# Kernel optimization log

Measured on AMD Instinct MI355X. Metric: run time of the kernel, lower is better.

Reference implementation:

```python
import jax, jax.numpy as jnp
import numpy as np

B, S, D = 2, 2048, 768
H = 12
HD = D // H


def setup_inputs() -> dict:
    key = jax.random.key(0)
    ks = jax.random.split(key, 9)
    s_in = 1.0 / np.sqrt(D)
    return {
        "x": jax.random.normal(ks[0], (B, S, D), dtype=jnp.float32),
        "wq": jax.random.normal(ks[1], (D, D), dtype=jnp.float32) * s_in,
        "bq": jax.random.normal(ks[2], (D,), dtype=jnp.float32) * 0.01,
        "wk": jax.random.normal(ks[3], (D, D), dtype=jnp.float32) * s_in,
        "bk": jax.random.normal(ks[4], (D,), dtype=jnp.float32) * 0.01,
        "wv": jax.random.normal(ks[5], (D, D), dtype=jnp.float32) * s_in,
        "bv": jax.random.normal(ks[6], (D,), dtype=jnp.float32) * 0.01,
        "wo": jax.random.normal(ks[7], (D, D), dtype=jnp.float32) * s_in,
        "bo": jax.random.normal(ks[8], (D,), dtype=jnp.float32) * 0.01,
    }


def reference(x, wq, bq, wk, bk, wv, bv, wo, bo):
    b, s, _ = x.shape
    # projections -> [b, h, s, hd]
    def proj(w, bias):
        return (x @ w + bias).reshape(b, s, H, HD).transpose(0, 2, 1, 3)
    q = proj(wq, bq)
    k = proj(wk, bk)
    v = proj(wv, bv)
    scores = jnp.einsum("bhqd,bhkd->bhqk", q, k)
    causal = jnp.triu(jnp.ones((s, s), dtype=bool), k=1)
    scores = jnp.where(causal, -jnp.inf, scores)
    attn = jax.nn.softmax(scores / np.sqrt(HD), axis=-1)
    # dropout p=0.0 -> identity
    ctx = jnp.einsum("bhqk,bhkd->bhqd", attn, v)
    ctx = ctx.transpose(0, 2, 1, 3).reshape(b, s, D)
    return ctx @ wo + bo
```

## Files before the change

### kernel.cpp

```cpp
#include <hip/hip_runtime.h>
#include <math.h>

#define BB  2
#define SS  2048
#define DD  768
#define HH  12
#define HDD 64
#define BSR (BB * SS)
#define NQT (SS / 64)

typedef __attribute__((ext_vector_type(8))) short bf16x8;
typedef __attribute__((ext_vector_type(4))) float f32x4;
typedef __attribute__((ext_vector_type(4))) int  i32x4;

__device__ inline f32x4 mfma16(bf16x8 a, bf16x8 b, f32x4 c) {
    return __builtin_amdgcn_mfma_f32_16x16x32_bf16(a, b, c, 0, 0, 0);
}

__device__ inline unsigned short f2b(float f) {
    unsigned int u = __float_as_uint(f);
    u += 0x7FFFu + ((u >> 16) & 1u);
    return (unsigned short)(u >> 16);
}
__device__ inline float b2f(unsigned short u) {
    return __uint_as_float((unsigned int)u << 16);
}

__device__ inline void async_copy16(void* lds, const void* g) {
    __builtin_amdgcn_global_load_lds(
        (const __attribute__((address_space(1))) unsigned int*)g,
        (__attribute__((address_space(3))) unsigned int*)lds, 16, 0, 0);
}

__global__ __launch_bounds__(256) void conv_x_kernel(
    const float* __restrict__ x, unsigned short* __restrict__ xb)
{
    int id = blockIdx.x * 256 + threadIdx.x;
    size_t base = (size_t)id * 8;
    float4 a = *(const float4*)&x[base];
    float4 b = *(const float4*)&x[base + 4];
    unsigned short o[8] = {f2b(a.x), f2b(a.y), f2b(a.z), f2b(a.w),
                           f2b(b.x), f2b(b.y), f2b(b.z), f2b(b.w)};
    *(i32x4*)&xb[base] = *(const i32x4*)o;
}

__global__ __launch_bounds__(256) void conv_wT_kernel(
    const float* __restrict__ w0, const float* __restrict__ w1,
    const float* __restrict__ w2, const float* __restrict__ w3,
    unsigned short* __restrict__ o0, unsigned short* __restrict__ o1,
    unsigned short* __restrict__ o2, unsigned short* __restrict__ o3)
{
    const float* w = (blockIdx.z == 0) ? w0 : (blockIdx.z == 1) ? w1
                   : (blockIdx.z == 2) ? w2 : w3;
    unsigned short* o = (blockIdx.z == 0) ? o0 : (blockIdx.z == 1) ? o1
                      : (blockIdx.z == 2) ? o2 : o3;
    const int n0 = blockIdx.x * 64;
    const int k0 = blockIdx.y * 64;
    const int tid = threadIdx.x;

    __shared__ unsigned short tile[64][72];

#pragma unroll
    for (int p = 0; p < 4; ++p) {
        int c  = p * 256 + tid;
        int kr = c >> 4;
        int nc = (c & 15) * 4;
        float4 v = *(const float4*)&w[(size_t)(k0 + kr) * DD + n0 + nc];
        tile[nc + 0][kr] = f2b(v.x);
        tile[nc + 1][kr] = f2b(v.y);
        tile[nc + 2][kr] = f2b(v.z);
        tile[nc + 3][kr] = f2b(v.w);
    }
    __syncthreads();
#pragma unroll
    for (int p = 0; p < 2; ++p) {
        int c  = p * 256 + tid;
        int nr = c >> 3;
        int kc = (c & 7) * 8;
        *(i32x4*)&o[(size_t)(n0 + nr) * DD + k0 + kc] = *(const i32x4*)&tile[nr][kc];
    }
}

__device__ inline void mainloop_64x128(
    const unsigned short* __restrict__ A, const unsigned short* __restrict__ Bt,
    unsigned short (*As)[64], unsigned short (*Bs)[64],
    f32x4 acc[2][4], int m0, int n0, int tid, int mh, int nh, int l16, int quad)
{
    const int swz = l16 & 7;
    for (int k0 = 0; k0 < DD; k0 += 64) {
        __syncthreads();
#pragma unroll
        for (int p = 0; p < 2; ++p) {
            int c  = p * 256 + tid;
            int r  = c >> 3;
            int ch = (c & 7) ^ (r & 7);
            async_copy16(&As[r][(c & 7) * 8], &A[(size_t)(m0 + r) * DD + k0 + ch * 8]);
        }
#pragma unroll
        for (int p = 0; p < 4; ++p) {
            int c  = p * 256 + tid;
            int r  = c >> 3;
            int ch = (c & 7) ^ (r & 7);
            async_copy16(&Bs[r][(c & 7) * 8], &Bt[(size_t)(n0 + r) * DD + k0 + ch * 8]);
        }
        __syncthreads();
        bf16x8 af0[2], af1[2], bf0[4], bf1[4];
#pragma unroll
        for (int mt = 0; mt < 2; ++mt) {
            int r = mh * 32 + mt * 16 + l16;
            af0[mt] = *(const bf16x8*)&As[r][((quad    ) ^ swz) * 8];
            af1[mt] = *(const bf16x8*)&As[r][((quad + 4) ^ swz) * 8];
        }
#pragma unroll
        for (int nt = 0; nt < 4; ++nt) {
            int r = nh * 64 + nt * 16 + l16;
            bf0[nt] = *(const bf16x8*)&Bs[r][((quad    ) ^ swz) * 8];
            bf1[nt] = *(const bf16x8*)&Bs[r][((quad + 4) ^ swz) * 8];
        }
#pragma unroll
        for (int mt = 0; mt < 2; ++mt)
#pragma unroll
            for (int nt = 0; nt < 4; ++nt) {
                acc[mt][nt] = mfma16(af0[mt], bf0[nt], acc[mt][nt]);
                acc[mt][nt] = mfma16(af1[mt], bf1[nt], acc[mt][nt]);
            }
    }
}

__global__ __launch_bounds__(256) void qkv_gemm_kernel(
    const unsigned short* __restrict__ xb,
    const unsigned short* __restrict__ wqT, const unsigned short* __restrict__ wkT,
    const unsigned short* __restrict__ wvT,
    const float* __restrict__ bq, const float* __restrict__ bk,
    const float* __restrict__ bv,
    unsigned short* __restrict__ Qg, unsigned short* __restrict__ Kg,
    unsigned short* __restrict__ Vg)
{
    const int which = blockIdx.z;
    const unsigned short* Bt = (which == 0) ? wqT : (which == 1) ? wkT : wvT;
    const float* bias        = (which == 0) ? bq  : (which == 1) ? bk  : bv;
    unsigned short* out      = (which == 0) ? Qg  : (which == 1) ? Kg  : Vg;

    const int m0 = blockIdx.x * 64;
    const int n0 = blockIdx.y * 128;
    const int tid  = threadIdx.x;
    const int w    = tid >> 6;
    const int lane = tid & 63;
    const int quad = lane >> 4;
    const int l16  = lane & 15;
    const int mh   = w & 1;
    const int nh   = w >> 1;

    __shared__ unsigned short smem[12288];
    unsigned short (*As)[64]  = (unsigned short(*)[64])smem;
    unsigned short (*Bs)[64]  = (unsigned short(*)[64])(smem + 4096);
    unsigned short (*T)[136]  = (unsigned short(*)[136])smem;

    f32x4 zero = {0.f, 0.f, 0.f, 0.f};
    f32x4 acc[2][4];
#pragma unroll
    for (int i = 0; i < 2; ++i)
#pragma unroll
        for (int j = 0; j < 4; ++j) acc[i][j] = zero;

    mainloop_64x128(xb, Bt, As, Bs, acc, m0, n0, tid, mh, nh, l16, quad);

    __syncthreads();

    if (which < 2) {
#pragma unroll
        for (int nt = 0; nt < 4; ++nt) {
            const int col = nh * 64 + nt * 16 + l16;
            const float bvv = bias[n0 + col];
#pragma unroll
            for (int mt = 0; mt < 2; ++mt)
#pragma unroll
                for (int r = 0; r < 4; ++r)
                    T[mh * 32 + mt * 16 + quad * 4 + r][col] =
                        f2b(acc[mt][nt][r] + bvv);
        }
        __syncthreads();
#pragma unroll
        for (int p2 = 0; p2 < 4; ++p2) {
            int c    = p2 * 256 + tid;
            int row  = c >> 4;
            int ck   = c & 15;
            int head = ck >> 3;
            int wi   = ck & 7;
            int sg   = m0 + row;
            int bi   = sg >> 11, si = sg & 2047;
            int hcol = (n0 >> 6) + head;
            *(i32x4*)&out[(((size_t)(bi * HH + hcol)) * SS + si) * HDD + wi * 8] =
                *(const i32x4*)&T[row][head * 64 + wi * 8];
        }
    } else {
        for (int pass = 0; pass < 2; ++pass) {
            if (pass) __syncthreads();
            if (nh == pass) {
#pragma unroll
                for (int nt = 0; nt < 4; ++nt) {
                    const float bvv = bias[n0 + pass * 64 + nt * 16 + l16];
#pragma unroll
                    for (int mt = 0; mt < 2; ++mt) {
                        ushort4 pk;
                        pk.x = f2b(acc[mt][nt][0] + bvv);
                        pk.y = f2b(acc[mt][nt][1] + bvv);
                        pk.z = f2b(acc[mt][nt][2] + bvv);
                        pk.w = f2b(acc[mt][nt][3] + bvv);
                        *(ushort4*)&T[nt * 16 + l16][mh * 32 + mt * 16 + quad * 4] = pk;
                    }
                }
            }
            __syncthreads();
            const int bi   = m0 >> 11;
            const int s0   = m0 & 2047;
            const int hcol = (n0 >> 6) + pass;
#pragma unroll
            for (int p2 = 0; p2 < 2; ++p2) {
                int c    = p2 * 256 + tid;
                int drow = c >> 3;
                int wi   = c & 7;
                *(i32x4*)&out[(((size_t)(bi * HH + hcol)) * HDD + drow) * SS + s0 + wi * 8] =
                    *(const i32x4*)&T[drow][wi * 8];
            }
        }
    }
}

__global__ __launch_bounds__(256) void out_gemm_kernel(
    const unsigned short* __restrict__ cb, const unsigned short* __restrict__ woT,
    const float* __restrict__ bo, float* __restrict__ out)
{
    const int m0 = blockIdx.x * 64;
    const int n0 = blockIdx.y * 128;
    const int tid  = threadIdx.x;
    const int w    = tid >> 6;
    const int lane = tid & 63;
    const int quad = lane >> 4;
    const int l16  = lane & 15;
    const int mh   = w & 1;
    const int nh   = w >> 1;

    __shared__ unsigned short As[64][64];
    __shared__ unsigned short Bs[128][64];

    f32x4 zero = {0.f, 0.f, 0.f, 0.f};
    f32x4 acc[2][4];
#pragma unroll
    for (int i = 0; i < 2; ++i)
#pragma unroll
        for (int j = 0; j < 4; ++j) acc[i][j] = zero;

    mainloop_64x128(cb, woT, As, Bs, acc, m0, n0, tid, mh, nh, l16, quad);

#pragma unroll
    for (int nt = 0; nt < 4; ++nt) {
        const int n = n0 + nh * 64 + nt * 16 + l16;
        const float bvv = bo[n];
#pragma unroll
        for (int mt = 0; mt < 2; ++mt) {
            const int mbase = m0 + mh * 32 + mt * 16 + quad * 4;
#pragma unroll
            for (int r = 0; r < 4; ++r)
                out[(size_t)(mbase + r) * DD + n] = acc[mt][nt][r] + bvv;
        }
    }
}

__global__ __launch_bounds__(256, 3) void attn_mfma_kernel(
    const unsigned short* __restrict__ Qg, const unsigned short* __restrict__ Kg,
    const unsigned short* __restrict__ Vg, unsigned short* __restrict__ Opart,
    float* __restrict__ Mb, float* __restrict__ Lb)
{
    const int sp = blockIdx.x & 1;
    const int qt = (NQT - 1) - (blockIdx.x >> 1);
    const int h  = blockIdx.y;
    const int b  = blockIdx.z;
    const int tid  = threadIdx.x;
    const int w    = tid >> 6;
    const int lane = tid & 63;
    const int quad = lane >> 4;
    const int l16  = lane & 15;
    const int q0   = qt * 64;

    const size_t bh = (size_t)(b * HH + h);
    const unsigned short* qp = Qg + bh * SS * HDD;
    const unsigned short* kp = Kg + bh * SS * HDD;
    const unsigned short* vp = Vg + bh * HDD * SS;

    unsigned short* op = Opart + ((size_t)sp * BB * HH + bh) * SS * HDD;
    float* mp = Mb + ((size_t)sp * BB * HH + bh) * SS;
    float* lp = Lb + ((size_t)sp * BB * HH + bh) * SS;

    const int nT  = qt + 1;
    const int mid = (nT + 1) >> 1;
    const int lo  = sp ? mid : 0;
    const int hi  = sp ? nT  : mid;

    const int query = q0 + w * 16 + l16;

    if (lo >= hi) {
        if (quad == 0) { mp[query] = -INFINITY; lp[query] = 0.f; }
        i32x4 z4 = {0, 0, 0, 0};
#pragma unroll
        for (int p2 = 0; p2 < 2; ++p2) {
            int c = p2 * 64 + lane;
            int row = c >> 3, dc = c & 7;
            *(i32x4*)&op[(size_t)(q0 + w * 16 + row) * HDD + dc * 8] = z4;
        }
        return;
    }

    __shared__ unsigned short Ks[2][64][72];
    __shared__ unsigned short Vt[2][64][72];
    __shared__ unsigned short PsT[4][16][72];
    unsigned short* slab = &PsT[w][0][0];

    const bf16x8 qb0 = *(const bf16x8*)&qp[(size_t)query * HDD + quad * 8];
    const bf16x8 qb1 = *(const bf16x8*)&qp[(size_t)query * HDD + 32 + quad * 8];

    const int pr = tid >> 3;
    const int po = (tid & 7) * 8;

    i32x4 kpre[2], vpre[2];
#pragma unroll
    for (int p = 0; p < 2; ++p) {
        int r = pr + p * 32;
        kpre[p] = *(const i32x4*)&kp[(size_t)(lo * 64 + r) * HDD + po];
        vpre[p] = *(const i32x4*)&vp[(size_t)r * SS + lo * 64 + po];
    }
#pragma unroll
    for (int p = 0; p < 2; ++p) {
        int r = pr + p * 32;
        *(i32x4*)&Ks[0][r][po] = kpre[p];
        *(i32x4*)&Vt[0][r][po] = vpre[p];
    }
    if (lo + 1 < hi) {
#pragma unroll
        for (int p = 0; p < 2; ++p) {
            int r = pr + p * 32;
            kpre[p] = *(const i32x4*)&kp[(size_t)((lo + 1) * 64 + r) * HDD + po];
            vpre[p] = *(const i32x4*)&vp[(size_t)r * SS + (lo + 1) * 64 + po];
        }
    }

    f32x4 zero = {0.f, 0.f, 0.f, 0.f};
    f32x4 o_acc[4];
    float m_i = -INFINITY, l_i = 0.f;
#pragma unroll
    for (int i = 0; i < 4; ++i) o_acc[i] = zero;

    for (int kt = lo; kt < hi; ++kt) {
        const int cbuf = (kt - lo) & 1;
        const int k0   = kt * 64;
        __syncthreads();

        if (kt + 1 < hi) {
#pragma unroll
            for (int p = 0; p < 2; ++p) {
                int r = pr + p * 32;
                *(i32x4*)&Ks[cbuf ^ 1][r][po] = kpre[p];
                *(i32x4*)&Vt[cbuf ^ 1][r][po] = vpre[p];
            }
        }
        if (kt + 2 < hi) {
            const int kn = (kt + 2) * 64;
#pragma unroll
            for (int p = 0; p < 2; ++p) {
                int r = pr + p * 32;
                kpre[p] = *(const i32x4*)&kp[(size_t)(kn + r) * HDD + po];
                vpre[p] = *(const i32x4*)&vp[(size_t)r * SS + kn + po];
            }
        }

        f32x4 s_acc[4];
#pragma unroll
        for (int t = 0; t < 4; ++t) {
            bf16x8 klo = *(const bf16x8*)&Ks[cbuf][t * 16 + l16][quad * 8];
            bf16x8 khi = *(const bf16x8*)&Ks[cbuf][t * 16 + l16][32 + quad * 8];
            s_acc[t] = mfma16(klo, qb0, zero);
            s_acc[t] = mfma16(khi, qb1, s_acc[t]);
        }

        float ps[4][4];
        float mx = -INFINITY;
#pragma unroll
        for (int t = 0; t < 4; ++t)
#pragma unroll
            for (int r = 0; r < 4; ++r) {
                const int key = k0 + t * 16 + quad * 4 + r;
                float val = s_acc[t][r] * 0.125f;
                if (kt == qt && key > query) val = -INFINITY;
                ps[t][r] = val;
                mx = fmaxf(mx, val);
            }
        mx = fmaxf(mx, __shfl_xor(mx, 16));
        mx = fmaxf(mx, __shfl_xor(mx, 32));
        const float mnew  = fmaxf(m_i, mx);
        const float alpha = __expf(m_i - mnew);
        float lsum = 0.f;
#pragma unroll
        for (int t = 0; t < 4; ++t)
#pragma unroll
            for (int r = 0; r < 4; ++r) {
                float pv = __expf(ps[t][r] - mnew);
                ps[t][r] = pv;
                lsum += pv;
            }
        lsum += __shfl_xor(lsum, 16);
        lsum += __shfl_xor(lsum, 32);
        l_i = l_i * alpha + lsum;
        m_i = mnew;
#pragma unroll
        for (int t = 0; t < 4; ++t)
#pragma unroll
            for (int r = 0; r < 4; ++r) o_acc[t][r] *= alpha;

#pragma unroll
        for (int t = 0; t < 4; ++t) {
            ushort4 pk;
            pk.x = f2b(ps[t][0]);
            pk.y = f2b(ps[t][1]);
            pk.z = f2b(ps[t][2]);
            pk.w = f2b(ps[t][3]);
            *(ushort4*)&slab[l16 * 72 + t * 16 + quad * 4] = pk;
        }
        bf16x8 pb0 = *(const bf16x8*)&slab[l16 * 72 + quad * 8];
        bf16x8 pb1 = *(const bf16x8*)&slab[l16 * 72 + 32 + quad * 8];

#pragma unroll
        for (int t2 = 0; t2 < 4; ++t2) {
            bf16x8 vlo = *(const bf16x8*)&Vt[cbuf][t2 * 16 + l16][quad * 8];
            bf16x8 vhi = *(const bf16x8*)&Vt[cbuf][t2 * 16 + l16][32 + quad * 8];
            o_acc[t2] = mfma16(vlo, pb0, o_acc[t2]);
            o_acc[t2] = mfma16(vhi, pb1, o_acc[t2]);
        }
    }

    if (quad == 0) { mp[query] = m_i; lp[query] = l_i; }
#pragma unroll
    for (int t2 = 0; t2 < 4; ++t2) {
        ushort4 pk;
        pk.x = f2b(o_acc[t2][0]);
        pk.y = f2b(o_acc[t2][1]);
        pk.z = f2b(o_acc[t2][2]);
        pk.w = f2b(o_acc[t2][3]);
        *(ushort4*)&slab[l16 * 72 + t2 * 16 + quad * 4] = pk;
    }
#pragma unroll
    for (int p2 = 0; p2 < 2; ++p2) {
        int c   = p2 * 64 + lane;
        int row = c >> 3, dc = c & 7;
        *(i32x4*)&op[(size_t)(q0 + w * 16 + row) * HDD + dc * 8] =
            *(const i32x4*)&slab[row * 72 + dc * 8];
    }
}

__global__ __launch_bounds__(256) void merge_kernel(
    const unsigned short* __restrict__ Opart, const float* __restrict__ Mb,
    const float* __restrict__ Lb, unsigned short* __restrict__ cb)
{
    const int qt  = blockIdx.x;
    const int bhn = blockIdx.y;
    const int b   = bhn / HH, h = bhn % HH;
    const int tid = threadIdx.x;
    const int row = tid >> 2;
    const int d0  = (tid & 3) * 16;
    const int q   = qt * 64 + row;

    const size_t base0 = (size_t)bhn * SS;
    const size_t base1 = ((size_t)BB * HH + bhn) * SS;

    float m0 = Mb[base0 + q], m1 = Mb[base1 + q];
    float l0 = Lb[base0 + q], l1 = Lb[base1 + q];
    float M  = fmaxf(m0, m1);
    float w0 = __expf(m0 - M), w1 = __expf(m1 - M);
    float inv = 1.0f / (w0 * l0 + w1 * l1);
    w0 *= inv; w1 *= inv;

    const unsigned short* o0 = Opart + (base0 + q) * HDD + d0;
    const unsigned short* o1 = Opart + (base1 + q) * HDD + d0;
    unsigned short res[16];
#pragma unroll
    for (int i = 0; i < 16; ++i)
        res[i] = f2b(w0 * b2f(o0[i]) + w1 * b2f(o1[i]));
    unsigned short* dst = &cb[((size_t)(b * SS + q)) * DD + h * HDD + d0];
    *(i32x4*)&dst[0] = *(const i32x4*)&res[0];
    *(i32x4*)&dst[8] = *(const i32x4*)&res[8];
}

extern "C" void kernel_launch(void* const* d_in, const int* in_sizes, int n_in,
                              void* d_out, int out_size, void* d_ws, size_t ws_size,
                              hipStream_t stream)
{
    const float* x  = (const float*)d_in[0];
    const float* wq = (const float*)d_in[1];
    const float* bq = (const float*)d_in[2];
    const float* wk = (const float*)d_in[3];
    const float* bk = (const float*)d_in[4];
    const float* wv = (const float*)d_in[5];
    const float* bv = (const float*)d_in[6];
    const float* wo = (const float*)d_in[7];
    const float* bo = (const float*)d_in[8];
    float* out = (float*)d_out;

    char* p = (char*)d_ws;
    const size_t XB = (size_t)BSR * DD * 2;
    const size_t WB = (size_t)DD * DD * 2;
    const size_t MLB = (size_t)2 * BB * HH * SS * 4;
    unsigned short* xb  = (unsigned short*)p;            p += XB;
    unsigned short* wqT = (unsigned short*)p;            p += WB;
    unsigned short* wkT = (unsigned short*)p;            p += WB;
    unsigned short* wvT = (unsigned short*)p;            p += WB;
    unsigned short* woT = (unsigned short*)p;            p += WB;
    unsigned short* Qg  = (unsigned short*)p;            p += XB;
    unsigned short* Kg  = (unsigned short*)p;            p += XB;
    unsigned short* Vg  = (unsigned short*)p;            p += XB;
    unsigned short* cb  = (unsigned short*)p;            p += XB;
    unsigned short* Opart = (unsigned short*)p;          p += 2 * XB;
    float* Mb = (float*)p;                               p += MLB;
    float* Lb = (float*)p;                               p += MLB;

    conv_x_kernel<<<BSR * DD / (256 * 8), 256, 0, stream>>>(x, xb);
    conv_wT_kernel<<<dim3(DD / 64, DD / 64, 4), 256, 0, stream>>>(
        wq, wk, wv, wo, wqT, wkT, wvT, woT);
    qkv_gemm_kernel<<<dim3(BSR / 64, DD / 128, 3), 256, 0, stream>>>(
        xb, wqT, wkT, wvT, bq, bk, bv, Qg, Kg, Vg);
    attn_mfma_kernel<<<dim3(NQT * 2, HH, BB), 256, 0, stream>>>(
        Qg, Kg, Vg, Opart, Mb, Lb);
    merge_kernel<<<dim3(NQT, BB * HH), 256, 0, stream>>>(Opart, Mb, Lb, cb);
    out_gemm_kernel<<<dim3(BSR / 64, DD / 128), 256, 0, stream>>>(cb, woT, bo, out);
}
```

Baseline: 181.0 us.

## Single-buffer swizzled K/V LDS tiles, fold softmax scale into Q, raise occupancy

The attention kernel's K/V shared-memory tiles become single-buffered with an XOR swizzle instead of padded double buffers. This shrinks LDS use so the launch bound can request 6 blocks per CU instead of 3. The 1/sqrt(hd) scale moves into the Q projection epilogue, removing a multiply per score. The cost is an extra barrier per key tile and prefetch only one tile ahead, so more latency must be hidden by the extra occupancy, and Q is now rounded to bf16 after scaling.

```diff
diff --git a/kernel.cpp b/kernel.cpp
--- a/kernel.cpp
+++ b/kernel.cpp
@@ -140,6 +140,7 @@
     const unsigned short* Bt = (which == 0) ? wqT : (which == 1) ? wkT : wvT;
     const float* bias        = (which == 0) ? bq  : (which == 1) ? bk  : bv;
     unsigned short* out      = (which == 0) ? Qg  : (which == 1) ? Kg  : Vg;
+    const float qs           = (which == 0) ? 0.125f : 1.0f;
 
     const int m0 = blockIdx.x * 64;
     const int n0 = blockIdx.y * 128;
@@ -177,7 +178,7 @@
 #pragma unroll
                 for (int r = 0; r < 4; ++r)
                     T[mh * 32 + mt * 16 + quad * 4 + r][col] =
-                        f2b(acc[mt][nt][r] + bvv);
+                        f2b((acc[mt][nt][r] + bvv) * qs);
         }
         __syncthreads();
 #pragma unroll
@@ -267,7 +268,7 @@
     }
 }
 
-__global__ __launch_bounds__(256, 3) void attn_mfma_kernel(
+__global__ __launch_bounds__(256, 6) void attn_mfma_kernel(
     const unsigned short* __restrict__ Qg, const unsigned short* __restrict__ Kg,
     const unsigned short* __restrict__ Vg, unsigned short* __restrict__ Opart,
     float* __restrict__ Mb, float* __restrict__ Lb)
@@ -311,37 +312,25 @@
         return;
     }
 
-    __shared__ unsigned short Ks[2][64][72];
-    __shared__ unsigned short Vt[2][64][72];
+    __shared__ unsigned short Ks[64][64];
+    __shared__ unsigned short Vt[64][64];
     __shared__ unsigned short PsT[4][16][72];
     unsigned short* slab = &PsT[w][0][0];
 
     const bf16x8 qb0 = *(const bf16x8*)&qp[(size_t)query * HDD + quad * 8];
     const bf16x8 qb1 = *(const bf16x8*)&qp[(size_t)query * HDD + 32 + quad * 8];
 
-    const int pr = tid >> 3;
-    const int po = (tid & 7) * 8;
+    const int pr  = tid >> 3;
+    const int po8 = tid & 7;
+    const int fs  = l16 & 7;
 
     i32x4 kpre[2], vpre[2];
 #pragma unroll
     for (int p = 0; p < 2; ++p) {
-        int r = pr + p * 32;
-        kpre[p] = *(const i32x4*)&kp[(size_t)(lo * 64 + r) * HDD + po];
-        vpre[p] = *(const i32x4*)&vp[(size_t)r * SS + lo * 64 + po];
-    }
-#pragma unroll
-    for (int p = 0; p < 2; ++p) {
-        int r = pr + p * 32;
-        *(i32x4*)&Ks[0][r][po] = kpre[p];
-        *(i32x4*)&Vt[0][r][po] = vpre[p];
-    }
-    if (lo + 1 < hi) {
-#pragma unroll
-        for (int p = 0; p < 2; ++p) {
-            int r = pr + p * 32;
-            kpre[p] = *(const i32x4*)&kp[(size_t)((lo + 1) * 64 + r) * HDD + po];
-            vpre[p] = *(const i32x4*)&vp[(size_t)r * SS + (lo + 1) * 64 + po];
-        }
+        int r  = pr + p * 32;
+        int gc = (po8 ^ (r & 7)) * 8;
+        kpre[p] = *(const i32x4*)&kp[(size_t)(lo * 64 + r) * HDD + gc];
+        vpre[p] = *(const i32x4*)&vp[(size_t)r * SS + lo * 64 + gc];
     }
 
     f32x4 zero = {0.f, 0.f, 0.f, 0.f};
@@ -351,33 +340,33 @@
     for (int i = 0; i < 4; ++i) o_acc[i] = zero;
 
     for (int kt = lo; kt < hi; ++kt) {
-        const int cbuf = (kt - lo) & 1;
-        const int k0   = kt * 64;
+        const int k0 = kt * 64;
         __syncthreads();
+#pragma unroll
+        for (int p = 0; p < 2; ++p) {
+            int r = pr + p * 32;
+            *(i32x4*)&Ks[r][po8 * 8] = kpre[p];
+            *(i32x4*)&Vt[r][po8 * 8] = vpre[p];
+        }
+        __syncthreads();
 
         if (kt + 1 < hi) {
+            const int kn = (kt + 1) * 64;
 #pragma unroll
             for (int p = 0; p < 2; ++p) {
-                int r = pr + p * 32;
-                *(i32x4*)&Ks[cbuf ^ 1][r][po] = kpre[p];
-                *(i32x4*)&Vt[cbuf ^ 1][r][po] = vpre[p];
+                int r  = pr + p * 32;
+                int gc = (po8 ^ (r & 7)) * 8;
+                kpre[p] = *(const i32x4*)&kp[(size_t)(kn + r) * HDD + gc];
+                vpre[p] = *(const i32x4*)&vp[(size_t)r * SS + kn + gc];
             }
         }
-        if (kt + 2 < hi) {
-            const int kn = (kt + 2) * 64;
-#pragma unroll
-            for (int p = 0; p < 2; ++p) {
-                int r = pr + p * 32;
-                kpre[p] = *(const i32x4*)&kp[(size_t)(kn + r) * HDD + po];
-                vpre[p] = *(const i32x4*)&vp[(size_t)r * SS + kn + po];
-            }
-        }
 
         f32x4 s_acc[4];
 #pragma unroll
         for (int t = 0; t < 4; ++t) {
-            bf16x8 klo = *(const bf16x8*)&Ks[cbuf][t * 16 + l16][quad * 8];
-            bf16x8 khi = *(const bf16x8*)&Ks[cbuf][t * 16 + l16][32 + quad * 8];
+            const int row = t * 16 + l16;
+            bf16x8 klo = *(const bf16x8*)&Ks[row][((quad    ) ^ fs) * 8];
+            bf16x8 khi = *(const bf16x8*)&Ks[row][((quad + 4) ^ fs) * 8];
             s_acc[t] = mfma16(klo, qb0, zero);
             s_acc[t] = mfma16(khi, qb1, s_acc[t]);
         }
@@ -389,7 +378,7 @@
 #pragma unroll
             for (int r = 0; r < 4; ++r) {
                 const int key = k0 + t * 16 + quad * 4 + r;
-                float val = s_acc[t][r] * 0.125f;
+                float val = s_acc[t][r];
                 if (kt == qt && key > query) val = -INFINITY;
                 ps[t][r] = val;
                 mx = fmaxf(mx, val);
@@ -430,8 +419,9 @@
 
 #pragma unroll
         for (int t2 = 0; t2 < 4; ++t2) {
-            bf16x8 vlo = *(const bf16x8*)&Vt[cbuf][t2 * 16 + l16][quad * 8];
-            bf16x8 vhi = *(const bf16x8*)&Vt[cbuf][t2 * 16 + l16][32 + quad * 8];
+            const int row = t2 * 16 + l16;
+            bf16x8 vlo = *(const bf16x8*)&Vt[row][((quad    ) ^ fs) * 8];
+            bf16x8 vhi = *(const bf16x8*)&Vt[row][((quad + 4) ^ fs) * 8];
             o_acc[t2] = mfma16(vlo, pb0, o_acc[t2]);
             o_acc[t2] = mfma16(vhi, pb1, o_acc[t2]);
         }
```

Measured after the change: 216.4 us. +19.6%, slower.
